# Kernel tuning notes

Hardware: AMD Instinct MI355X
Metric: run time of the kernel (lower is better)

The kernel has to match this reference:

```python
import jax, jax.numpy as jnp
import numpy as np

CUTOFF = 100.0
SR = 16000.0
Q = 0.7071067811865476  # 1/sqrt(2), torchaudio default
BATCH, T = 64, 480000


def _biquad_coeffs():
    # RBJ highpass biquad coefficients, normalized by a0
    w0 = 2.0 * np.pi * CUTOFF / SR
    alpha = np.sin(w0) / (2.0 * Q)
    cosw = np.cos(w0)
    b0 = (1.0 + cosw) / 2.0
    b1 = -(1.0 + cosw)
    b2 = b0
    a0 = 1.0 + alpha
    a1 = -2.0 * cosw
    a2 = 1.0 - alpha
    return tuple(float(c / a0) for c in (b0, b1, b2, a1, a2))


def setup_inputs() -> dict:
    key = jax.random.key(0)
    audio = jax.random.normal(key, (BATCH, T), dtype=jnp.float32)
    return {"audio": audio}


def reference(audio):
    # audio: [B, T]; order-2 IIR (Direct Form I) recurrence along time
    b0, b1, b2, a1, a2 = _biquad_coeffs()

    def step(carry, x):
        x1, x2, y1, y2 = carry  # each [B]
        y = b0 * x + b1 * x1 + b2 * x2 - a1 * y1 - a2 * y2
        return (x, x1, y, y1), y

    B = audio.shape[0]
    z = jnp.zeros((B,), audio.dtype)
    _, ys = jax.lax.scan(step, (z, z, z, z), audio.T)  # ys: [T, B]
    return ys.T
```

## Files before the change

kernel.cpp:

```cpp
#include <hip/hip_runtime.h>
#include <cmath>

#define T_LEN 480000
#define BATCH 64
#define L     64
#define WARMT 6
#define OUTT  (256 - WARMT)
#define SPB   (OUTT * L)
#define BPR   (T_LEN / SPB)

#define STEP(xi, yo) do {                                   \
    float f_  = fmaf(b0, (xi), fmaf(b1, x1, b2 * x2));      \
    float g_  = fmaf(c2, y2, f_);                           \
    float yy_ = fmaf(c1, y1, g_);                           \
    x2 = x1; x1 = (xi);                                     \
    y2 = y1; y1 = yy_;                                      \
    (yo) = yy_;                                             \
} while (0)

__global__ __launch_bounds__(256, 4) void highpass_kernel(
    const float* __restrict__ in, float* __restrict__ out,
    const float b0, const float b1, const float b2,
    const float c1, const float c2,
    const float4 M1, const float4 M2, const float4 M3,
    const float4 M4, const float4 M5)
{
    const int r = blockIdx.x / BPR;
    const int b = blockIdx.x - r * BPR;
    const int t = threadIdx.x;
    const size_t rowoff = (size_t)r * T_LEN;
    const int start = b * SPB + (t - WARMT) * L;

    float4 v[16];
    float pa = 0.f, pb = 0.f;
    float xs1 = 0.f, xs2 = 0.f;

    const bool active = (start >= 0);
    if (active) {
        if (start > 0) {
            xs1 = in[rowoff + start - 1];
            xs2 = in[rowoff + start - 2];
        }
        const float4* __restrict__ xv = (const float4*)(in + rowoff + start);
#pragma unroll
        for (int i = 0; i < 16; ++i) v[i] = xv[i];
        float x1 = xs1, x2 = xs2, y1 = 0.f, y2 = 0.f;
#pragma unroll
        for (int i = 0; i < 16; ++i) {
            float d;
            STEP(v[i].x, d); STEP(v[i].y, d); STEP(v[i].z, d); STEP(v[i].w, d);
        }
        pa = y1; pb = y2;
    }

    __shared__ float2 pl[256];
    pl[t] = make_float2(pa, pb);
    __syncthreads();
    if (t < WARMT) return;

    const float2 q1 = pl[t - 1], q2 = pl[t - 2], q3 = pl[t - 3],
                 q4 = pl[t - 4], q5 = pl[t - 5], q6 = pl[t - 6];
    float Y1 = q1.x, Y2 = q1.y;
    Y1 = fmaf(M1.x, q2.x, fmaf(M1.y, q2.y, Y1));
    Y2 = fmaf(M1.z, q2.x, fmaf(M1.w, q2.y, Y2));
    Y1 = fmaf(M2.x, q3.x, fmaf(M2.y, q3.y, Y1));
    Y2 = fmaf(M2.z, q3.x, fmaf(M2.w, q3.y, Y2));
    Y1 = fmaf(M3.x, q4.x, fmaf(M3.y, q4.y, Y1));
    Y2 = fmaf(M3.z, q4.x, fmaf(M3.w, q4.y, Y2));
    Y1 = fmaf(M4.x, q5.x, fmaf(M4.y, q5.y, Y1));
    Y2 = fmaf(M4.z, q5.x, fmaf(M4.w, q5.y, Y2));
    Y1 = fmaf(M5.x, q6.x, fmaf(M5.y, q6.y, Y1));
    Y2 = fmaf(M5.z, q6.x, fmaf(M5.w, q6.y, Y2));

    {
        float x1 = xs1, x2 = xs2, y1 = Y1, y2 = Y2;
#pragma unroll
        for (int i = 0; i < 16; ++i) {
            float4 q;
            STEP(v[i].x, q.x); STEP(v[i].y, q.y);
            STEP(v[i].z, q.z); STEP(v[i].w, q.w);
            v[i] = q;
        }
    }

    float4* __restrict__ yv = (float4*)(out + rowoff + start);
#pragma unroll
    for (int i = 0; i < 16; ++i) yv[i] = v[i];
}

static void matmul2(const double* a, const double* bm, double* o) {
    o[0] = a[0]*bm[0] + a[1]*bm[2];
    o[1] = a[0]*bm[1] + a[1]*bm[3];
    o[2] = a[2]*bm[0] + a[3]*bm[2];
    o[3] = a[2]*bm[1] + a[3]*bm[3];
}

extern "C" void kernel_launch(void* const* d_in, const int* in_sizes, int n_in,
                              void* d_out, int out_size, void* d_ws, size_t ws_size,
                              hipStream_t stream) {
    const float* in  = (const float*)d_in[0];
    float*       out = (float*)d_out;

    const double Q     = 0.7071067811865476;
    const double w0    = 2.0 * M_PI * 100.0 / 16000.0;
    const double alpha = sin(w0) / (2.0 * Q);
    const double cosw  = cos(w0);
    const double b0d = (1.0 + cosw) / 2.0;
    const double b1d = -(1.0 + cosw);
    const double b2d = b0d;
    const double a0d = 1.0 + alpha;
    const double c1d = -(-2.0 * cosw) / a0d;
    const double c2d = -(1.0 - alpha) / a0d;

    double A[4] = {c1d, c2d, 1.0, 0.0};
    double M[4] = {A[0], A[1], A[2], A[3]};
    for (int s = 0; s < 6; ++s) {
        double tmp[4]; matmul2(M, M, tmp);
        M[0]=tmp[0]; M[1]=tmp[1]; M[2]=tmp[2]; M[3]=tmp[3];
    }
    double P[5][4];
    P[0][0]=M[0]; P[0][1]=M[1]; P[0][2]=M[2]; P[0][3]=M[3];
    for (int k = 1; k < 5; ++k) matmul2(P[k-1], M, P[k]);

    float4 Mv[5];
    for (int k = 0; k < 5; ++k)
        Mv[k] = make_float4((float)P[k][0], (float)P[k][1],
                            (float)P[k][2], (float)P[k][3]);

    const float b0 = (float)(b0d / a0d);
    const float b1 = (float)(b1d / a0d);
    const float b2 = (float)(b2d / a0d);
    const float c1 = (float)c1d;
    const float c2 = (float)c2d;

    const int grid = BATCH * BPR;
    hipLaunchKernelGGL(highpass_kernel, dim3(grid), dim3(256), 0, stream,
                       in, out, b0, b1, b2, c1, c2,
                       Mv[0], Mv[1], Mv[2], Mv[3], Mv[4]);
}
```

Baseline: 234.5 us.

## Replace second IIR pass with superposition of zero-state output and impulse-response correction

The first pass now keeps the zero-initial-state outputs for all 64 samples. The true output is then formed as that partial output plus Y1*U[n] + Y2*W[n], where U and W are the homogeneous responses tabulated at compile time. This replaces the second serial 64-step recurrence with independent FMAs, and turning the coefficients into constexpr values lets them be folded as immediates. The cost is more live registers (the full p[16] array across the barrier) and slightly different float rounding.

```diff
diff --git a/kernel.cpp b/kernel.cpp
--- a/kernel.cpp
+++ b/kernel.cpp
@@ -8,6 +8,31 @@
 #define OUTT  (256 - WARMT)
 #define SPB   (OUTT * L)
 #define BPR   (T_LEN / SPB)
+
+constexpr double kPI = 3.14159265358979323846;
+constexpr double csin(double x){ double t=x,s=x; for(int i=1;i<14;++i){ t*=-x*x/double((2*i)*(2*i+1)); s+=t;} return s; }
+constexpr double ccos(double x){ double t=1,s=1; for(int i=1;i<14;++i){ t*=-x*x/double((2*i-1)*(2*i)); s+=t;} return s; }
+
+struct Tab { float U[L]; float W[L]; float b0,b1,b2,c1,c2; };
+constexpr Tab make_tab(){
+    Tab t{};
+    const double w0    = 2.0*kPI*100.0/16000.0;
+    const double alpha = csin(w0)/(2.0*0.7071067811865476);
+    const double cw    = ccos(w0);
+    const double a0    = 1.0+alpha;
+    const double b0 = (1.0+cw)/2.0/a0, b1 = -(1.0+cw)/a0, b2 = b0;
+    const double c1 = 2.0*cw/a0;
+    const double c2 = -(1.0-alpha)/a0;
+    t.b0=(float)b0; t.b1=(float)b1; t.b2=(float)b2; t.c1=(float)c1; t.c2=(float)c2;
+    double u1=1.0,u2=0.0,w1=0.0,w2=1.0;
+    for(int n=0;n<L;++n){
+        const double u = c1*u1 + c2*u2, w = c1*w1 + c2*w2;
+        t.U[n]=(float)u; t.W[n]=(float)w;
+        u2=u1; u1=u; w2=w1; w1=w;
+    }
+    return t;
+}
+constexpr Tab TAB = make_tab();
 
 #define STEP(xi, yo) do {                                   \
     float f_  = fmaf(b0, (xi), fmaf(b1, x1, b2 * x2));      \
@@ -20,35 +45,38 @@
 
 __global__ __launch_bounds__(256, 4) void highpass_kernel(
     const float* __restrict__ in, float* __restrict__ out,
-    const float b0, const float b1, const float b2,
-    const float c1, const float c2,
     const float4 M1, const float4 M2, const float4 M3,
     const float4 M4, const float4 M5)
 {
+    constexpr float b0=TAB.b0, b1=TAB.b1, b2=TAB.b2, c1=TAB.c1, c2=TAB.c2;
+
     const int r = blockIdx.x / BPR;
     const int b = blockIdx.x - r * BPR;
     const int t = threadIdx.x;
     const size_t rowoff = (size_t)r * T_LEN;
     const int start = b * SPB + (t - WARMT) * L;
 
-    float4 v[16];
+    float4 p[16];
     float pa = 0.f, pb = 0.f;
-    float xs1 = 0.f, xs2 = 0.f;
 
     const bool active = (start >= 0);
     if (active) {
+        float xs1 = 0.f, xs2 = 0.f;
         if (start > 0) {
             xs1 = in[rowoff + start - 1];
             xs2 = in[rowoff + start - 2];
         }
         const float4* __restrict__ xv = (const float4*)(in + rowoff + start);
+        float4 v[16];
 #pragma unroll
         for (int i = 0; i < 16; ++i) v[i] = xv[i];
         float x1 = xs1, x2 = xs2, y1 = 0.f, y2 = 0.f;
 #pragma unroll
         for (int i = 0; i < 16; ++i) {
-            float d;
-            STEP(v[i].x, d); STEP(v[i].y, d); STEP(v[i].z, d); STEP(v[i].w, d);
+            float4 q;
+            STEP(v[i].x, q.x); STEP(v[i].y, q.y);
+            STEP(v[i].z, q.z); STEP(v[i].w, q.w);
+            p[i] = q;
         }
         pa = y1; pb = y2;
     }
@@ -72,20 +100,16 @@
     Y1 = fmaf(M5.x, q6.x, fmaf(M5.y, q6.y, Y1));
     Y2 = fmaf(M5.z, q6.x, fmaf(M5.w, q6.y, Y2));
 
-    {
-        float x1 = xs1, x2 = xs2, y1 = Y1, y2 = Y2;
-#pragma unroll
-        for (int i = 0; i < 16; ++i) {
-            float4 q;
-            STEP(v[i].x, q.x); STEP(v[i].y, q.y);
-            STEP(v[i].z, q.z); STEP(v[i].w, q.w);
-            v[i] = q;
-        }
-    }
-
     float4* __restrict__ yv = (float4*)(out + rowoff + start);
 #pragma unroll
-    for (int i = 0; i < 16; ++i) yv[i] = v[i];
+    for (int i = 0; i < 16; ++i) {
+        float4 q = p[i];
+        q.x = fmaf(Y1, TAB.U[4*i+0], fmaf(Y2, TAB.W[4*i+0], q.x));
+        q.y = fmaf(Y1, TAB.U[4*i+1], fmaf(Y2, TAB.W[4*i+1], q.y));
+        q.z = fmaf(Y1, TAB.U[4*i+2], fmaf(Y2, TAB.W[4*i+2], q.z));
+        q.w = fmaf(Y1, TAB.U[4*i+3], fmaf(Y2, TAB.W[4*i+3], q.w));
+        yv[i] = q;
+    }
 }
 
 static void matmul2(const double* a, const double* bm, double* o) {
@@ -105,11 +129,8 @@
     const double w0    = 2.0 * M_PI * 100.0 / 16000.0;
     const double alpha = sin(w0) / (2.0 * Q);
     const double cosw  = cos(w0);
-    const double b0d = (1.0 + cosw) / 2.0;
-    const double b1d = -(1.0 + cosw);
-    const double b2d = b0d;
     const double a0d = 1.0 + alpha;
-    const double c1d = -(-2.0 * cosw) / a0d;
+    const double c1d = 2.0 * cosw / a0d;
     const double c2d = -(1.0 - alpha) / a0d;
 
     double A[4] = {c1d, c2d, 1.0, 0.0};
@@ -127,14 +148,7 @@
         Mv[k] = make_float4((float)P[k][0], (float)P[k][1],
                             (float)P[k][2], (float)P[k][3]);
 
-    const float b0 = (float)(b0d / a0d);
-    const float b1 = (float)(b1d / a0d);
-    const float b2 = (float)(b2d / a0d);
-    const float c1 = (float)c1d;
-    const float c2 = (float)c2d;
-
     const int grid = BATCH * BPR;
     hipLaunchKernelGGL(highpass_kernel, dim3(grid), dim3(256), 0, stream,
-                       in, out, b0, b1, b2, c1, c2,
-                       Mv[0], Mv[1], Mv[2], Mv[3], Mv[4]);
+                       in, out, Mv[0], Mv[1], Mv[2], Mv[3], Mv[4]);
 }
```

After: 245.6 us. 4.7% more time.
